# Performance work log

Measured on AMD Instinct MI355X. Metric: run time of the kernel, lower is better.

## Reference

```python
import jax, jax.numpy as jnp
import numpy as np

NUM_MODELS = 16
NUM_CLASSES = 17929
HIDDEN = 4
BATCH = 512


def setup_inputs() -> dict:
    key = jax.random.key(0)
    k1, k2, k3, k4, k5 = jax.random.split(key, 5)
    x = jax.random.normal(k1, (NUM_MODELS, BATCH, NUM_CLASSES), dtype=jnp.float32)
    # stacked per-class Linear(num_models, hidden) weights/biases
    W1 = jax.random.normal(k2, (NUM_CLASSES, HIDDEN, NUM_MODELS), dtype=jnp.float32) * 0.1
    b1 = jax.random.normal(k3, (NUM_CLASSES, HIDDEN), dtype=jnp.float32) * 0.1
    # stacked per-class Linear(hidden, 1) weights (squeezed) / biases
    W2 = jax.random.normal(k4, (NUM_CLASSES, HIDDEN), dtype=jnp.float32) * 0.1
    b2 = jax.random.normal(k5, (NUM_CLASSES,), dtype=jnp.float32) * 0.1
    return {"x": x, "W1": W1, "b1": b1, "W2": W2, "b2": b2}


def reference(x, W1, b1, W2, b2):
    # x: [M, B, C] -> permute(1, 2, 0) -> [B, C, M]
    xp = jnp.transpose(x, (1, 2, 0))
    # per-class first Linear + ReLU: h[b,c,h] = relu(sum_m xp[b,c,m] * W1[c,h,m] + b1[c,h])
    h = jax.nn.relu(jnp.einsum('bcm,chm->bch', xp, W1) + b1[None, :, :])
    # per-class second Linear(hidden -> 1), concatenated over classes -> [B, C]
    out = jnp.einsum('bch,ch->bc', h, W2) + b2[None, :]
    return out
```

## Files before the change

### kernel.cpp

```cpp
#include <hip/hip_runtime.h>


#define NUM_MODELS 16
#define HIDDEN 4
#define BATCH 512
#define NUM_CLASSES 17929
#define KB 16
#define CT 256

__global__ __launch_bounds__(CT) void FamilyMLPLinear_kernel(
    const float* __restrict__ x,
    const float* __restrict__ W1,
    const float* __restrict__ b1,
    const float* __restrict__ W2,
    const float* __restrict__ b2,
    float* __restrict__ out)
{
    const int c = blockIdx.x * CT + threadIdx.x;
    if (c >= NUM_CLASSES) return;
    const int b0 = blockIdx.y * KB;

    float w1[HIDDEN][NUM_MODELS];
    const float4* W1v = (const float4*)(W1 + (size_t)c * (HIDDEN * NUM_MODELS));
    #pragma unroll
    for (int j = 0; j < HIDDEN; ++j) {
        #pragma unroll
        for (int q = 0; q < NUM_MODELS / 4; ++q) {
            float4 v = W1v[j * (NUM_MODELS / 4) + q];
            w1[j][q * 4 + 0] = v.x;
            w1[j][q * 4 + 1] = v.y;
            w1[j][q * 4 + 2] = v.z;
            w1[j][q * 4 + 3] = v.w;
        }
    }
    const float4 b1v = *(const float4*)(b1 + (size_t)c * HIDDEN);
    const float bias1[HIDDEN] = {b1v.x, b1v.y, b1v.z, b1v.w};
    const float4 w2v = *(const float4*)(W2 + (size_t)c * HIDDEN);
    const float w2[HIDDEN] = {w2v.x, w2v.y, w2v.z, w2v.w};
    const float bias2 = b2[c];

    const size_t BC = (size_t)BATCH * NUM_CLASSES;

    #pragma unroll 1
    for (int bi = 0; bi < KB; ++bi) {
        const int b = b0 + bi;
        const float* xp = x + (size_t)b * NUM_CLASSES + c;

        float xv[NUM_MODELS];
        #pragma unroll
        for (int m = 0; m < NUM_MODELS; ++m)
            xv[m] = xp[(size_t)m * BC];

        float acc = bias2;
        #pragma unroll
        for (int j = 0; j < HIDDEN; ++j) {
            float h = bias1[j];
            #pragma unroll
            for (int m = 0; m < NUM_MODELS; ++m)
                h = fmaf(xv[m], w1[j][m], h);
            h = fmaxf(h, 0.0f);
            acc = fmaf(h, w2[j], acc);
        }
        out[(size_t)b * NUM_CLASSES + c] = acc;
    }
}

extern "C" void kernel_launch(void* const* d_in, const int* in_sizes, int n_in,
                              void* d_out, int out_size, void* d_ws, size_t ws_size,
                              hipStream_t stream) {
    const float* x  = (const float*)d_in[0];
    const float* W1 = (const float*)d_in[1];
    const float* b1 = (const float*)d_in[2];
    const float* W2 = (const float*)d_in[3];
    const float* b2 = (const float*)d_in[4];
    float* out = (float*)d_out;

    dim3 grid((NUM_CLASSES + CT - 1) / CT, BATCH / KB);
    FamilyMLPLinear_kernel<<<grid, CT, 0, stream>>>(x, W1, b1, W2, b2, out);
}
```

Measured before the change: 772.5 us.

## Stage W1 in shared memory and process four classes per thread with vector loads

W1 for a 256-class block is now staged once into padded shared memory. Each thread handles four adjacent classes using 16-byte vector loads of x and stores of out, and the grid shrinks to 16 batch groups of 32 rows. The aim is to cut redundant per-thread W1 register loads across batch blocks and to widen global memory transactions on the bandwidth-bound x stream. In exchange it adds 68 KB of LDS per block, which limits occupancy, and a scalar fallback path for the tail classes.

```diff
diff --git a/kernel.cpp b/kernel.cpp
--- a/kernel.cpp
+++ b/kernel.cpp
@@ -1,14 +1,25 @@
 #include <hip/hip_runtime.h>
 
 
-#define NUM_MODELS 16
-#define HIDDEN 4
-#define BATCH 512
-#define NUM_CLASSES 17929
-#define KB 16
-#define CT 256
+#define NM 16
+#define NH 4
+#define NB 512
+#define NC 17929
+#define CBK 256
+#define ROWS 68
+#define GY 16
+#define BPB (NB / GY)
 
-__global__ __launch_bounds__(CT) void FamilyMLPLinear_kernel(
+typedef float f4 __attribute__((ext_vector_type(4)));
+
+__device__ __forceinline__ f4 load4(const float* p) {
+    f4 r; __builtin_memcpy(&r, p, 16); return r;
+}
+__device__ __forceinline__ void store4(float* p, f4 v) {
+    __builtin_memcpy(p, &v, 16);
+}
+
+__global__ __launch_bounds__(256) void FamilyMLPLinear_kernel(
     const float* __restrict__ x,
     const float* __restrict__ W1,
     const float* __restrict__ b1,
@@ -16,52 +27,110 @@
     const float* __restrict__ b2,
     float* __restrict__ out)
 {
-    const int c = blockIdx.x * CT + threadIdx.x;
-    if (c >= NUM_CLASSES) return;
-    const int b0 = blockIdx.y * KB;
+    __shared__ float w1s[CBK * ROWS];
 
-    float w1[HIDDEN][NUM_MODELS];
-    const float4* W1v = (const float4*)(W1 + (size_t)c * (HIDDEN * NUM_MODELS));
-    #pragma unroll
-    for (int j = 0; j < HIDDEN; ++j) {
+    const int tid = threadIdx.x;
+    const int cb  = blockIdx.x * CBK;
+
+    {
+        const float* src = W1 + (size_t)cb * (NH * NM);
+        const int nclass = min(CBK, NC - cb);
         #pragma unroll
-        for (int q = 0; q < NUM_MODELS / 4; ++q) {
-            float4 v = W1v[j * (NUM_MODELS / 4) + q];
-            w1[j][q * 4 + 0] = v.x;
-            w1[j][q * 4 + 1] = v.y;
-            w1[j][q * 4 + 2] = v.z;
-            w1[j][q * 4 + 3] = v.w;
+        for (int k = 0; k < 16; ++k) {
+            const int f  = tid + 256 * k;
+            const int i  = f >> 4;
+            const int kk = f & 15;
+            if (i < nclass) {
+                f4 v = load4(src + (size_t)i * (NH * NM) + 4 * kk);
+                const int r = (i >> 2) + (i & 3) * 64;
+                *(f4*)&w1s[r * ROWS + 4 * kk] = v;
+            }
         }
     }
-    const float4 b1v = *(const float4*)(b1 + (size_t)c * HIDDEN);
-    const float bias1[HIDDEN] = {b1v.x, b1v.y, b1v.z, b1v.w};
-    const float4 w2v = *(const float4*)(W2 + (size_t)c * HIDDEN);
-    const float w2[HIDDEN] = {w2v.x, w2v.y, w2v.z, w2v.w};
-    const float bias2 = b2[c];
 
-    const size_t BC = (size_t)BATCH * NUM_CLASSES;
+    const int q  = tid & 63;
+    const int bs = tid >> 6;
+    const int lc = q << 2;
+    const int cq = cb + lc;
+
+    f4 b1v[4], w2v[4];
+    float b2v[4];
+    #pragma unroll
+    for (int cls = 0; cls < 4; ++cls) {
+        const int c = cq + cls;
+        if (c < NC) {
+            b1v[cls] = load4(b1 + (size_t)c * NH);
+            w2v[cls] = load4(W2 + (size_t)c * NH);
+            b2v[cls] = b2[c];
+        } else {
+            f4 z = {0.f, 0.f, 0.f, 0.f};
+            b1v[cls] = z; w2v[cls] = z; b2v[cls] = 0.f;
+        }
+    }
+
+    __syncthreads();
+
+    const bool fullquad = (cq + 3 < NC);
+    const int b_base = blockIdx.y * BPB + bs;
+    const size_t MS = (size_t)NB * NC;
 
     #pragma unroll 1
-    for (int bi = 0; bi < KB; ++bi) {
-        const int b = b0 + bi;
-        const float* xp = x + (size_t)b * NUM_CLASSES + c;
+    for (int it = 0; it < BPB / 4; ++it) {
+        const int b = b_base + 4 * it;
 
-        float xv[NUM_MODELS];
-        #pragma unroll
-        for (int m = 0; m < NUM_MODELS; ++m)
-            xv[m] = xp[(size_t)m * BC];
+        if (fullquad) {
+            f4 xq[NM];
+            const float* xb = x + (size_t)b * NC + cq;
+            #pragma unroll
+            for (int m = 0; m < NM; ++m)
+                xq[m] = load4(xb + (size_t)m * MS);
 
-        float acc = bias2;
-        #pragma unroll
-        for (int j = 0; j < HIDDEN; ++j) {
-            float h = bias1[j];
+            f4 accv;
             #pragma unroll
-            for (int m = 0; m < NUM_MODELS; ++m)
-                h = fmaf(xv[m], w1[j][m], h);
-            h = fmaxf(h, 0.0f);
-            acc = fmaf(h, w2[j], acc);
+            for (int cls = 0; cls < 4; ++cls) {
+                const f4* wrow = (const f4*)&w1s[(q + (cls << 6)) * ROWS];
+                float acc = b2v[cls];
+                #pragma unroll
+                for (int j = 0; j < NH; ++j) {
+                    float h = b1v[cls][j];
+                    #pragma unroll
+                    for (int t = 0; t < 4; ++t) {
+                        f4 w = wrow[j * 4 + t];
+                        h = fmaf(xq[4 * t + 0][cls], w[0], h);
+                        h = fmaf(xq[4 * t + 1][cls], w[1], h);
+                        h = fmaf(xq[4 * t + 2][cls], w[2], h);
+                        h = fmaf(xq[4 * t + 3][cls], w[3], h);
+                    }
+                    h = fmaxf(h, 0.f);
+                    acc = fmaf(h, w2v[cls][j], acc);
+                }
+                accv[cls] = acc;
+            }
+            store4(out + (size_t)b * NC + cq, accv);
+        } else {
+            #pragma unroll
+            for (int cls = 0; cls < 4; ++cls) {
+                const int c = cq + cls;
+                if (c >= NC) break;
+                const float* xb = x + (size_t)b * NC + c;
+                float xv[NM];
+                #pragma unroll
+                for (int m = 0; m < NM; ++m)
+                    xv[m] = xb[(size_t)m * MS];
+                const float* wrow = &w1s[(q + (cls << 6)) * ROWS];
+                float acc = b2v[cls];
+                #pragma unroll
+                for (int j = 0; j < NH; ++j) {
+                    float h = b1v[cls][j];
+                    #pragma unroll
+                    for (int m = 0; m < NM; ++m)
+                        h = fmaf(xv[m], wrow[j * NM + m], h);
+                    h = fmaxf(h, 0.f);
+                    acc = fmaf(h, w2v[cls][j], acc);
+                }
+                out[(size_t)b * NC + c] = acc;
+            }
         }
-        out[(size_t)b * NUM_CLASSES + c] = acc;
     }
 }
 
@@ -75,6 +144,6 @@
     const float* b2 = (const float*)d_in[4];
     float* out = (float*)d_out;
 
-    dim3 grid((NUM_CLASSES + CT - 1) / CT, BATCH / KB);
-    FamilyMLPLinear_kernel<<<grid, CT, 0, stream>>>(x, W1, b1, W2, b2, out);
+    dim3 grid((NC + CBK - 1) / CBK, GY);
+    FamilyMLPLinear_kernel<<<grid, 256, 0, stream>>>(x, W1, b1, W2, b2, out);
 }
```

New measurement: 778.9 us. No clear change (+0.8%).
